# Performance work log

Measured on AMD Instinct MI355X. Metric: run time of the kernel, lower is better.

Reference implementation:

```python
import jax, jax.numpy as jnp
import numpy as np
import math

B, T, C, H = 2, 2048, 1024, 16
D = C // H
EPS = 1e-5

def _layer_norm(x, w, b):
    m = jnp.mean(x, axis=-1, keepdims=True)
    v = jnp.mean((x - m) ** 2, axis=-1, keepdims=True)
    return (x - m) * jax.lax.rsqrt(v + EPS) * w + b

def setup_inputs() -> dict:
    key = jax.random.key(0)
    ks = jax.random.split(key, 8)
    s_attn = 1.0 / math.sqrt(C)
    s_fc = 1.0 / math.sqrt(C)
    s_fc2 = 1.0 / math.sqrt(4 * C)
    return {
        "x": jax.random.normal(ks[0], (B, T, C), dtype=jnp.float32),
        "ln1_w": jnp.ones((C,), jnp.float32),
        "ln1_b": jnp.zeros((C,), jnp.float32),
        "w_qkv": jax.random.normal(ks[1], (C, 3 * C), jnp.float32) * s_attn,  # [in,out]
        "b_qkv": jnp.zeros((3 * C,), jnp.float32),
        "w_proj": jax.random.normal(ks[2], (C, C), jnp.float32) * s_attn,
        "b_proj": jnp.zeros((C,), jnp.float32),
        "ln2_w": jnp.ones((C,), jnp.float32),
        "ln2_b": jnp.zeros((C,), jnp.float32),
        "w_fc": jax.random.normal(ks[3], (C, 4 * C), jnp.float32) * s_fc,
        "b_fc": jnp.zeros((4 * C,), jnp.float32),
        "w_fc2": jax.random.normal(ks[4], (4 * C, C), jnp.float32) * s_fc2,
        "b_fc2": jnp.zeros((C,), jnp.float32),
    }

def reference(x, ln1_w, ln1_b, w_qkv, b_qkv, w_proj, b_proj,
              ln2_w, ln2_b, w_fc, b_fc, w_fc2, b_fc2):
    # --- attention branch ---
    h = _layer_norm(x, ln1_w, ln1_b)
    qkv = h @ w_qkv + b_qkv                      # [B,T,3C]
    q, k, v = jnp.split(qkv, 3, axis=-1)
    # [B,T,C] -> [B,H,T,D]
    q = q.reshape(B, T, H, D).transpose(0, 2, 1, 3)
    k = k.reshape(B, T, H, D).transpose(0, 2, 1, 3)
    v = v.reshape(B, T, H, D).transpose(0, 2, 1, 3)
    scale = 1.0 / math.sqrt(D)
    scores = jnp.einsum("bhtd,bhsd->bhts", q, k) * scale  # [B,H,T,T]
    causal = jnp.tril(jnp.ones((T, T), dtype=bool))
    scores = jnp.where(causal, scores, -jnp.inf)
    attn_w = jax.nn.softmax(scores, axis=-1)     # dropout_p = 0.0
    attn_out = jnp.einsum("bhts,bhsd->bhtd", attn_w, v)
    attn_out = attn_out.transpose(0, 2, 1, 3).reshape(B, T, C)
    attn_out = attn_out @ w_proj + b_proj
    x = x + attn_out
    # --- MLP branch ---
    h2 = _layer_norm(x, ln2_w, ln2_b)
    h2 = jax.nn.gelu(h2 @ w_fc + b_fc, approximate=False)
    x = x + (h2 @ w_fc2 + b_fc2)
    return x, jnp.mean(attn_w, axis=0)           # ([B,T,C], [H,T,T])
```

## Files before the change

### kernel.cpp

```cpp
#include <hip/hip_runtime.h>
#include <cmath>

#define BB 2
#define TT 2048
#define CC 1024
#define HH 16
#define DD 64

typedef unsigned short u16;
typedef __attribute__((ext_vector_type(8))) short bf16x8;
typedef __attribute__((ext_vector_type(4))) float f32x4;

__device__ __forceinline__ u16 f2bf(float f) {
    union { float f; unsigned u; } v; v.f = f;
    return (u16)((v.u + 0x7fff + ((v.u >> 16) & 1)) >> 16);
}

__device__ __forceinline__ float bf2f(u16 h) {
    union { unsigned u; float f; } v; v.u = ((unsigned)h) << 16;
    return v.f;
}

__device__ __forceinline__ float gelu_exact(float v) {
    return 0.5f * v * (1.0f + erff(v * 0.70710678118654752440f));
}

__device__ __forceinline__ void glds16(const void* g, void* l) {
    __builtin_amdgcn_global_load_lds(
        (const __attribute__((address_space(1))) void*)g,
        (__attribute__((address_space(3))) void*)l, 16, 0, 0);
}

__global__ __launch_bounds__(256) void wcvt_kernel(const float* __restrict__ W,
                                                   u16* __restrict__ WT,
                                                   int K, int N) {
    __shared__ u16 t[64][65];
    const int n0 = blockIdx.x * 64, k0 = blockIdx.y * 64;
    const int tid = threadIdx.x;
    const int c = tid & 63;
#pragma unroll
    for (int it = 0; it < 16; ++it) {
        int r = it * 4 + (tid >> 6);
        t[c][r] = f2bf(W[(size_t)(k0 + r) * N + n0 + c]);
    }
    __syncthreads();
#pragma unroll
    for (int it = 0; it < 16; ++it) {
        int r = it * 4 + (tid >> 6);
        WT[(size_t)(n0 + r) * K + k0 + c] = t[r][c];
    }
}

__global__ __launch_bounds__(256) void ln_kernel(const float* __restrict__ x,
                                                 const float* __restrict__ w,
                                                 const float* __restrict__ b,
                                                 u16* __restrict__ out) {
    const int row = blockIdx.x;
    const int tid = threadIdx.x;
    const float* xr = x + (size_t)row * CC;
    u16* orow = out + (size_t)row * CC;

    __shared__ float red[256];

    float v[4];
#pragma unroll
    for (int i = 0; i < 4; ++i) v[i] = xr[tid + i * 256];

    red[tid] = v[0] + v[1] + v[2] + v[3];
    __syncthreads();
    for (int off = 128; off > 0; off >>= 1) {
        if (tid < off) red[tid] += red[tid + off];
        __syncthreads();
    }
    const float mean = red[0] * (1.0f / CC);
    __syncthreads();

    float d[4], sq = 0.f;
#pragma unroll
    for (int i = 0; i < 4; ++i) { d[i] = v[i] - mean; sq += d[i] * d[i]; }
    red[tid] = sq;
    __syncthreads();
    for (int off = 128; off > 0; off >>= 1) {
        if (tid < off) red[tid] += red[tid + off];
        __syncthreads();
    }
    const float rstd = rsqrtf(red[0] * (1.0f / CC) + 1e-5f);

#pragma unroll
    for (int i = 0; i < 4; ++i) {
        int c = tid + i * 256;
        orow[c] = f2bf(d[i] * rstd * w[c] + b[c]);
    }
}

template <int EPI, int OUTBF, int WM, int WN, int FI, int FJ>
__global__ __launch_bounds__(256) void gemm_mfma(const u16* __restrict__ A,
                                                 const u16* __restrict__ BT,
                                                 const float* __restrict__ bias,
                                                 const float* __restrict__ res,
                                                 void* __restrict__ out,
                                                 int M, int N, int K) {
    constexpr int TM = WM * FI * 16;
    constexpr int TN = WN * FJ * 16;
    __shared__ u16 As[TM * 32];
    __shared__ u16 Bs[TN * 32];

    const int tid = threadIdx.x;
    const int lane = tid & 63;
    const int w = tid >> 6;
    const int wr = w / WN, wc = w % WN;
    const int m16 = lane & 15;
    const int quad = lane >> 4;

    const int bm = blockIdx.y * TM;
    const int bn = blockIdx.x * TN;

    f32x4 acc[FI][FJ] = {};

    for (int k0 = 0; k0 < K; k0 += 32) {
#pragma unroll
        for (int it = 0; it < TM / 64; ++it) {
            int cb = w * (TM / 64) * 64 + it * 64;
            int q = cb + lane;
            glds16(&A[(size_t)(bm + (q >> 2)) * K + k0 + (q & 3) * 8], &As[cb * 8]);
        }
#pragma unroll
        for (int it = 0; it < TN / 64; ++it) {
            int cb = w * (TN / 64) * 64 + it * 64;
            int q = cb + lane;
            glds16(&BT[(size_t)(bn + (q >> 2)) * K + k0 + (q & 3) * 8], &Bs[cb * 8]);
        }
        __syncthreads();

        bf16x8 a[FI], b[FJ];
#pragma unroll
        for (int i = 0; i < FI; ++i)
            a[i] = *(const bf16x8*)&As[(wr * FI * 16 + 16 * i + m16) * 32 + quad * 8];
#pragma unroll
        for (int j = 0; j < FJ; ++j)
            b[j] = *(const bf16x8*)&Bs[(wc * FJ * 16 + 16 * j + m16) * 32 + quad * 8];
#pragma unroll
        for (int i = 0; i < FI; ++i)
#pragma unroll
            for (int j = 0; j < FJ; ++j)
                acc[i][j] = __builtin_amdgcn_mfma_f32_16x16x32_bf16(a[i], b[j], acc[i][j], 0, 0, 0);
        __syncthreads();
    }

#pragma unroll
    for (int i = 0; i < FI; ++i) {
        const int row = bm + wr * FI * 16 + 16 * i + quad * 4;
#pragma unroll
        for (int j = 0; j < FJ; ++j) {
            const int col = bn + wc * FJ * 16 + 16 * j + m16;
            const float bv = bias[col];
#pragma unroll
            for (int r = 0; r < 4; ++r) {
                float v = acc[i][j][r] + bv;
                if (EPI == 1) v = gelu_exact(v);
                if (EPI == 2) v += res[(size_t)(row + r) * N + col];
                if (OUTBF) ((u16*)out)[(size_t)(row + r) * N + col] = f2bf(v);
                else ((float*)out)[(size_t)(row + r) * N + col] = v;
            }
        }
    }
}

__global__ __launch_bounds__(256) void attn_kernel(const float* __restrict__ qkv,
                                                   float* __restrict__ attn_mean,
                                                   u16* __restrict__ attn_out) {
    const int lid = blockIdx.x;
    const int u = lid & 255;
    const int h = u & 15;
    const int ta = u >> 4;
    const int tt = (lid < 256) ? ta : 31 - ta;
    const int t0 = tt * 64;

    const int tid = threadIdx.x;
    const int lane = tid & 63;
    const int w = tid >> 6;
    const int m16 = lane & 15;
    const int quad = lane >> 4;
    const size_t TC3 = 3 * CC;

    __shared__ u16 Qh[2][64][64];
    __shared__ u16 Ql[2][64][64];
    __shared__ u16 Kh[64][64];
    __shared__ u16 Kl[64][64];
    __shared__ u16 VT[64][64];
    __shared__ u16 Ps[64][64];

    const int arow = w * 16 + m16;
    const int sw = (m16 & 7) << 3;
    const int rbase = w * 16 + quad * 4;

    auto stage_hilo = [&](const float* src, u16 (*Hd)[64], u16 (*Ld)[64], float scale) {
#pragma unroll
        for (int it = 0; it < 4; ++it) {
            int e = tid + it * 256;
            int s = e >> 4, c4 = e & 15;
            float4 v = *reinterpret_cast<const float4*>(src + (size_t)s * TC3 + c4 * 4);
            float fv[4] = {v.x * scale, v.y * scale, v.z * scale, v.w * scale};
            u16 hh[4], ll[4];
#pragma unroll
            for (int i = 0; i < 4; ++i) {
                union { float f; unsigned u; } tbits; tbits.f = fv[i];
                hh[i] = (u16)(tbits.u >> 16);
                ll[i] = f2bf(fv[i] - bf2f(hh[i]));
            }
            int col = (c4 * 4) ^ ((s & 7) << 3);
            *reinterpret_cast<ushort4*>(&Hd[s][col]) = make_ushort4(hh[0], hh[1], hh[2], hh[3]);
            *reinterpret_cast<ushort4*>(&Ld[s][col]) = make_ushort4(ll[0], ll[1], ll[2], ll[3]);
        }
    };

    auto stage_vt = [&](const float* src) {
#pragma unroll
        for (int it = 0; it < 4; ++it) {
            int e = tid + it * 256;
            int s = e >> 4, c4 = e & 15;
            float4 v = *reinterpret_cast<const float4*>(src + (size_t)s * TC3 + c4 * 4);
            float fv[4] = {v.x, v.y, v.z, v.w};
#pragma unroll
            for (int i = 0; i < 4; ++i) {
                int d = c4 * 4 + i;
                VT[d][s ^ ((d & 7) << 3)] = f2bf(fv[i]);
            }
        }
    };

    auto compute_S = [&](int b, f32x4 (&acc)[4], bool diag) {
#pragma unroll
        for (int ks = 0; ks < 2; ++ks) {
            const int acol = (ks * 32 + quad * 8) ^ sw;
            bf16x8 ah = *(const bf16x8*)&Qh[b][arow][acol];
            bf16x8 al = *(const bf16x8*)&Ql[b][arow][acol];
#pragma unroll
            for (int j = 0; j < 4; ++j) {
                bf16x8 bh = *(const bf16x8*)&Kh[j * 16 + m16][acol];
                bf16x8 bl = *(const bf16x8*)&Kl[j * 16 + m16][acol];
                acc[j] = __builtin_amdgcn_mfma_f32_16x16x32_bf16(ah, bh, acc[j], 0, 0, 0);
                acc[j] = __builtin_amdgcn_mfma_f32_16x16x32_bf16(al, bh, acc[j], 0, 0, 0);
                acc[j] = __builtin_amdgcn_mfma_f32_16x16x32_bf16(ah, bl, acc[j], 0, 0, 0);
            }
        }
        if (diag) {
#pragma unroll
            for (int j = 0; j < 4; ++j)
#pragma unroll
                for (int r = 0; r < 4; ++r)
                    if (j * 16 + m16 > rbase + r) acc[j][r] = -INFINITY;
        }
    };

    auto pv_acc = [&](f32x4 (&O)[4]) {
#pragma unroll
        for (int ks = 0; ks < 2; ++ks) {
            const int ko = (ks * 32 + quad * 8) ^ sw;
            bf16x8 a = *(const bf16x8*)&Ps[arow][ko];
#pragma unroll
            for (int j = 0; j < 4; ++j) {
                bf16x8 bv = *(const bf16x8*)&VT[j * 16 + m16][ko];
                O[j] = __builtin_amdgcn_mfma_f32_16x16x32_bf16(a, bv, O[j], 0, 0, 0);
            }
        }
    };

    stage_hilo(qkv + (size_t)t0 * TC3 + h * DD, Qh[0], Ql[0], 0.125f);
    stage_hilo(qkv + (size_t)TT * TC3 + (size_t)t0 * TC3 + h * DD, Qh[1], Ql[1], 0.125f);

    float m_b[2][4], l_b[2][4];
#pragma unroll
    for (int b = 0; b < 2; ++b) {
        float m_r[4] = {-INFINITY, -INFINITY, -INFINITY, -INFINITY};
        float l_r[4] = {0.f, 0.f, 0.f, 0.f};
        const float* kbase = qkv + (size_t)b * TT * TC3 + CC + h * DD;
        for (int st = 0; st <= tt; ++st) {
            __syncthreads();
            stage_hilo(kbase + (size_t)st * 64 * TC3, Kh, Kl, 1.0f);
            __syncthreads();
            f32x4 acc[4] = {};
            compute_S(b, acc, st == tt);
#pragma unroll
            for (int r = 0; r < 4; ++r) {
                float t = fmaxf(fmaxf(acc[0][r], acc[1][r]), fmaxf(acc[2][r], acc[3][r]));
                t = fmaxf(t, __shfl_xor(t, 1));
                t = fmaxf(t, __shfl_xor(t, 2));
                t = fmaxf(t, __shfl_xor(t, 4));
                t = fmaxf(t, __shfl_xor(t, 8));
                const float mn = fmaxf(m_r[r], t);
                float sum = __expf(acc[0][r] - mn) + __expf(acc[1][r] - mn) +
                            __expf(acc[2][r] - mn) + __expf(acc[3][r] - mn);
                sum += __shfl_xor(sum, 1);
                sum += __shfl_xor(sum, 2);
                sum += __shfl_xor(sum, 4);
                sum += __shfl_xor(sum, 8);
                l_r[r] = l_r[r] * __expf(m_r[r] - mn) + sum;
                m_r[r] = mn;
            }
        }
#pragma unroll
        for (int r = 0; r < 4; ++r) { m_b[b][r] = m_r[r]; l_b[b][r] = 1.0f / l_r[r]; }
    }

    f32x4 O0[4] = {}, O1[4] = {};
    const float* k0base = qkv + CC + h * DD;
    const float* k1base = qkv + (size_t)TT * TC3 + CC + h * DD;
    const float* v0base = qkv + 2 * CC + h * DD;
    const float* v1base = qkv + (size_t)TT * TC3 + 2 * CC + h * DD;

    for (int st = 0; st <= tt; ++st) {
        const int s0 = st * 64;
        const bool diag = (st == tt);
        float P0[4][4], P1[4][4];

        __syncthreads();
        stage_hilo(k0base + (size_t)s0 * TC3, Kh, Kl, 1.0f);
        __syncthreads();
        {
            f32x4 acc[4] = {};
            compute_S(0, acc, diag);
#pragma unroll
            for (int j = 0; j < 4; ++j)
#pragma unroll
                for (int r = 0; r < 4; ++r)
                    P0[j][r] = __expf(acc[j][r] - m_b[0][r]) * l_b[0][r];
        }
        __syncthreads();
        stage_hilo(k1base + (size_t)s0 * TC3, Kh, Kl, 1.0f);
        __syncthreads();
        {
            f32x4 acc[4] = {};
            compute_S(1, acc, diag);
#pragma unroll
            for (int j = 0; j < 4; ++j)
#pragma unroll
                for (int r = 0; r < 4; ++r)
                    P1[j][r] = __expf(acc[j][r] - m_b[1][r]) * l_b[1][r];
        }
#pragma unroll
        for (int r = 0; r < 4; ++r) {
            float* mrow = attn_mean + ((size_t)h * TT + t0 + rbase + r) * TT + s0;
#pragma unroll
            for (int j = 0; j < 4; ++j)
                mrow[j * 16 + m16] = 0.5f * (P0[j][r] + P1[j][r]);
        }
#pragma unroll
        for (int r = 0; r < 4; ++r) {
            const int prow = rbase + r;
            const int psw = (prow & 7) << 3;
#pragma unroll
            for (int j = 0; j < 4; ++j)
                Ps[prow][(j * 16 + m16) ^ psw] = f2bf(P0[j][r]);
        }
        stage_vt(v0base + (size_t)s0 * TC3);
        __syncthreads();
        pv_acc(O0);
        __syncthreads();
#pragma unroll
        for (int r = 0; r < 4; ++r) {
            const int prow = rbase + r;
            const int psw = (prow & 7) << 3;
#pragma unroll
            for (int j = 0; j < 4; ++j)
                Ps[prow][(j * 16 + m16) ^ psw] = f2bf(P1[j][r]);
        }
        stage_vt(v1base + (size_t)s0 * TC3);
        __syncthreads();
        pv_acc(O1);
    }

#pragma unroll
    for (int r = 0; r < 4; ++r) {
        const int trow = t0 + rbase + r;
#pragma unroll
        for (int j = 0; j < 4; ++j) {
            attn_out[((size_t)0 * TT + trow) * CC + h * DD + j * 16 + m16] = f2bf(O0[j][r]);
            attn_out[((size_t)1 * TT + trow) * CC + h * DD + j * 16 + m16] = f2bf(O1[j][r]);
        }
    }

    const int c0 = (tt + 1) * 64;
    const float4 z4 = make_float4(0.f, 0.f, 0.f, 0.f);
    for (int r = 0; r < 64; ++r) {
        float* row = attn_mean + ((size_t)h * TT + t0 + r) * TT;
        for (int c = c0 + tid * 4; c < TT; c += 1024)
            *reinterpret_cast<float4*>(row + c) = z4;
    }
}

extern "C" void kernel_launch(void* const* d_in, const int* in_sizes, int n_in,
                              void* d_out, int out_size, void* d_ws, size_t ws_size,
                              hipStream_t stream) {
    const float* x      = (const float*)d_in[0];
    const float* ln1_w  = (const float*)d_in[1];
    const float* ln1_b  = (const float*)d_in[2];
    const float* w_qkv  = (const float*)d_in[3];
    const float* b_qkv  = (const float*)d_in[4];
    const float* w_proj = (const float*)d_in[5];
    const float* b_proj = (const float*)d_in[6];
    const float* ln2_w  = (const float*)d_in[7];
    const float* ln2_b  = (const float*)d_in[8];
    const float* w_fc   = (const float*)d_in[9];
    const float* b_fc   = (const float*)d_in[10];
    const float* w_fc2  = (const float*)d_in[11];
    const float* b_fc2  = (const float*)d_in[12];

    float* out_x    = (float*)d_out;
    float* out_attn = out_x + (size_t)BB * TT * CC;

    char* wp = (char*)d_ws;
    u16* wT_qkv = (u16*)wp;  wp += (size_t)3072 * 1024 * 2;
    u16* wT_proj = (u16*)wp; wp += (size_t)1024 * 1024 * 2;
    u16* wT_fc  = (u16*)wp;  wp += (size_t)4096 * 1024 * 2;
    u16* wT_fc2 = (u16*)wp;  wp += (size_t)1024 * 4096 * 2;
    u16* h_ln   = (u16*)wp;  wp += (size_t)4096 * 1024 * 2;
    u16* att_o  = (u16*)wp;  wp += (size_t)4096 * 1024 * 2;
    u16* h2     = (u16*)wp;  wp += (size_t)4096 * 4096 * 2;
    float* qkv  = (float*)wp; wp += (size_t)4096 * 3072 * 4;
    float* x1   = (float*)wp; wp += (size_t)4096 * 1024 * 4;

    const int M = BB * TT;

    wcvt_kernel<<<dim3(3072 / 64, 1024 / 64), 256, 0, stream>>>(w_qkv, wT_qkv, 1024, 3072);
    wcvt_kernel<<<dim3(1024 / 64, 1024 / 64), 256, 0, stream>>>(w_proj, wT_proj, 1024, 1024);
    wcvt_kernel<<<dim3(4096 / 64, 1024 / 64), 256, 0, stream>>>(w_fc, wT_fc, 1024, 4096);
    wcvt_kernel<<<dim3(1024 / 64, 4096 / 64), 256, 0, stream>>>(w_fc2, wT_fc2, 4096, 1024);

    ln_kernel<<<M, 256, 0, stream>>>(x, ln1_w, ln1_b, h_ln);
    gemm_mfma<0, 0, 2, 2, 4, 4><<<dim3(3072 / 128, M / 128), 256, 0, stream>>>(
        h_ln, wT_qkv, b_qkv, nullptr, qkv, M, 3072, 1024);
    attn_kernel<<<512, 256, 0, stream>>>(qkv, out_attn, att_o);
    gemm_mfma<2, 0, 4, 1, 2, 4><<<dim3(1024 / 64, M / 128), 256, 0, stream>>>(
        att_o, wT_proj, b_proj, x, x1, M, 1024, 1024);
    ln_kernel<<<M, 256, 0, stream>>>(x1, ln2_w, ln2_b, h_ln);
    gemm_mfma<1, 1, 2, 2, 4, 4><<<dim3(4096 / 128, M / 128), 256, 0, stream>>>(
        h_ln, wT_fc, b_fc, nullptr, h2, M, 4096, 1024);
    gemm_mfma<2, 0, 4, 1, 2, 4><<<dim3(1024 / 64, M / 128), 256, 0, stream>>>(
        h2, wT_fc2, b_fc2, x1, out_x, M, 1024, 4096);
}
```

Before: 788.4 us.

## Pre-convert K/V tiles to bf16 in a separate kernel and stream them via direct-to-LDS loads

New measurement: 719.0 us. 1.1x faster.

```diff
diff --git a/kernel.cpp b/kernel.cpp
--- a/kernel.cpp
+++ b/kernel.cpp
@@ -166,7 +166,61 @@
     }
 }
 
+__global__ __launch_bounds__(256) void qkvcvt_kernel(const float* __restrict__ qkv,
+                                                     u16* __restrict__ Khg,
+                                                     u16* __restrict__ Klg,
+                                                     u16* __restrict__ VTg) {
+    const int idx = blockIdx.x;
+    const int st = idx & 31;
+    const int h = (idx >> 5) & 15;
+    const int b = idx >> 9;
+    const int tid = threadIdx.x;
+    const size_t TC3 = 3 * CC;
+
+    const float* kbase = qkv + (size_t)b * TT * TC3 + (size_t)st * 64 * TC3 + CC + h * DD;
+    const float* vbase = kbase + CC;
+    u16* kh = Khg + (size_t)idx * 4096;
+    u16* kl = Klg + (size_t)idx * 4096;
+    u16* vt = VTg + (size_t)idx * 4096;
+
+    __shared__ u16 lvt[64][65];
+
+#pragma unroll
+    for (int it = 0; it < 4; ++it) {
+        int e = tid + it * 256;
+        int s = e >> 4, c4 = e & 15;
+        float4 v = *reinterpret_cast<const float4*>(kbase + (size_t)s * TC3 + c4 * 4);
+        float fv[4] = {v.x, v.y, v.z, v.w};
+        u16 hh[4], ll[4];
+#pragma unroll
+        for (int i = 0; i < 4; ++i) {
+            union { float f; unsigned u; } tb; tb.f = fv[i];
+            hh[i] = (u16)(tb.u >> 16);
+            ll[i] = f2bf(fv[i] - bf2f(hh[i]));
+        }
+        int col = (c4 * 4) ^ ((s & 7) << 3);
+        *reinterpret_cast<ushort4*>(&kh[s * 64 + col]) = make_ushort4(hh[0], hh[1], hh[2], hh[3]);
+        *reinterpret_cast<ushort4*>(&kl[s * 64 + col]) = make_ushort4(ll[0], ll[1], ll[2], ll[3]);
+        float4 vv = *reinterpret_cast<const float4*>(vbase + (size_t)s * TC3 + c4 * 4);
+        lvt[c4 * 4 + 0][s] = f2bf(vv.x);
+        lvt[c4 * 4 + 1][s] = f2bf(vv.y);
+        lvt[c4 * 4 + 2][s] = f2bf(vv.z);
+        lvt[c4 * 4 + 3][s] = f2bf(vv.w);
+    }
+    __syncthreads();
+#pragma unroll
+    for (int it = 0; it < 4; ++it) {
+        int e = tid + it * 256;
+        int d = e >> 4, s4 = (e & 15) * 4;
+        ushort4 o = make_ushort4(lvt[d][s4], lvt[d][s4 + 1], lvt[d][s4 + 2], lvt[d][s4 + 3]);
+        *reinterpret_cast<ushort4*>(&vt[d * 64 + (s4 ^ ((d & 7) << 3))]) = o;
+    }
+}
+
 __global__ __launch_bounds__(256) void attn_kernel(const float* __restrict__ qkv,
+                                                   const u16* __restrict__ Khg,
+                                                   const u16* __restrict__ Klg,
+                                                   const u16* __restrict__ VTg,
                                                    float* __restrict__ attn_mean,
                                                    u16* __restrict__ attn_out) {
     const int lid = blockIdx.x;
@@ -183,65 +237,58 @@
     const int quad = lane >> 4;
     const size_t TC3 = 3 * CC;
 
-    __shared__ u16 Qh[2][64][64];
-    __shared__ u16 Ql[2][64][64];
-    __shared__ u16 Kh[64][64];
-    __shared__ u16 Kl[64][64];
-    __shared__ u16 VT[64][64];
-    __shared__ u16 Ps[64][64];
+    __shared__ u16 Ks[2][2][64][64];
+    __shared__ u16 VTs[2][64][64];
 
     const int arow = w * 16 + m16;
     const int sw = (m16 & 7) << 3;
     const int rbase = w * 16 + quad * 4;
 
-    auto stage_hilo = [&](const float* src, u16 (*Hd)[64], u16 (*Ld)[64], float scale) {
-#pragma unroll
-        for (int it = 0; it < 4; ++it) {
-            int e = tid + it * 256;
-            int s = e >> 4, c4 = e & 15;
-            float4 v = *reinterpret_cast<const float4*>(src + (size_t)s * TC3 + c4 * 4);
-            float fv[4] = {v.x * scale, v.y * scale, v.z * scale, v.w * scale};
-            u16 hh[4], ll[4];
-#pragma unroll
-            for (int i = 0; i < 4; ++i) {
-                union { float f; unsigned u; } tbits; tbits.f = fv[i];
-                hh[i] = (u16)(tbits.u >> 16);
-                ll[i] = f2bf(fv[i] - bf2f(hh[i]));
-            }
-            int col = (c4 * 4) ^ ((s & 7) << 3);
-            *reinterpret_cast<ushort4*>(&Hd[s][col]) = make_ushort4(hh[0], hh[1], hh[2], hh[3]);
-            *reinterpret_cast<ushort4*>(&Ld[s][col]) = make_ushort4(ll[0], ll[1], ll[2], ll[3]);
-        }
+    auto toff = [&](int b, int st) -> size_t {
+        return ((size_t)((b * 16 + h) * 32 + st)) * 4096;
     };
 
-    auto stage_vt = [&](const float* src) {
-#pragma unroll
-        for (int it = 0; it < 4; ++it) {
-            int e = tid + it * 256;
-            int s = e >> 4, c4 = e & 15;
-            float4 v = *reinterpret_cast<const float4*>(src + (size_t)s * TC3 + c4 * 4);
-            float fv[4] = {v.x, v.y, v.z, v.w};
-#pragma unroll
-            for (int i = 0; i < 4; ++i) {
-                int d = c4 * 4 + i;
-                VT[d][s ^ ((d & 7) << 3)] = f2bf(fv[i]);
-            }
-        }
+    auto stage_tile = [&](const u16* g, u16* l) {
+        glds16(g + w * 1024 + lane * 8, l + w * 1024);
+        glds16(g + w * 1024 + 512 + lane * 8, l + w * 1024 + 512);
     };
 
-    auto compute_S = [&](int b, f32x4 (&acc)[4], bool diag) {
+    bf16x8 qh[2][2], ql[2][2];
+#pragma unroll
+    for (int b = 0; b < 2; ++b) {
+        const float* qp = qkv + (size_t)b * TT * TC3 + (size_t)(t0 + arow) * TC3 + h * DD;
 #pragma unroll
         for (int ks = 0; ks < 2; ++ks) {
-            const int acol = (ks * 32 + quad * 8) ^ sw;
-            bf16x8 ah = *(const bf16x8*)&Qh[b][arow][acol];
-            bf16x8 al = *(const bf16x8*)&Ql[b][arow][acol];
+            float4 v0 = *reinterpret_cast<const float4*>(qp + ks * 32 + quad * 8);
+            float4 v1 = *reinterpret_cast<const float4*>(qp + ks * 32 + quad * 8 + 4);
+            float f[8] = {v0.x, v0.y, v0.z, v0.w, v1.x, v1.y, v1.z, v1.w};
+            union { bf16x8 v; u16 s[8]; } H, L;
+#pragma unroll
+            for (int i = 0; i < 8; ++i) {
+                float fv = f[i] * 0.125f;
+                union { float f; unsigned u; } tb; tb.f = fv;
+                u16 hh = (u16)(tb.u >> 16);
+                H.s[i] = hh;
+                L.s[i] = f2bf(fv - bf2f(hh));
+            }
+            qh[b][ks] = H.v;
+            ql[b][ks] = L.v;
+        }
+    }
+
+    auto compute_S = [&](const bf16x8 (&QH)[2], const bf16x8 (&QL)[2],
+                         const u16 (*KH)[64], const u16 (*KL)[64],
+                         f32x4 (&acc)[4], bool diag) {
+#pragma unroll
+        for (int ks = 0; ks < 2; ++ks) {
 #pragma unroll
             for (int j = 0; j < 4; ++j) {
-                bf16x8 bh = *(const bf16x8*)&Kh[j * 16 + m16][acol];
-                bf16x8 bl = *(const bf16x8*)&Kl[j * 16 + m16][acol];
-                acc[j] = __builtin_amdgcn_mfma_f32_16x16x32_bf16(ah, bh, acc[j], 0, 0, 0);
-                acc[j] = __builtin_amdgcn_mfma_f32_16x16x32_bf16(al, bh, acc[j], 0, 0, 0);
-                acc[j] = __builtin_amdgcn_mfma_f32_16x16x32_bf16(ah, bl, acc[j], 0, 0, 0);
+                const int co = (ks * 32 + quad * 8) ^ sw;
+                bf16x8 bh = *(const bf16x8*)&KH[j * 16 + m16][co];
+                bf16x8 bl = *(const bf16x8*)&KL[j * 16 + m16][co];
+                acc[j] = __builtin_amdgcn_mfma_f32_16x16x32_bf16(QH[ks], bh, acc[j], 0, 0, 0);
+                acc[j] = __builtin_amdgcn_mfma_f32_16x16x32_bf16(QL[ks], bh, acc[j], 0, 0, 0);
+                acc[j] = __builtin_amdgcn_mfma_f32_16x16x32_bf16(QH[ks], bl, acc[j], 0, 0, 0);
             }
         }
         if (diag) {
@@ -253,34 +300,37 @@
         }
     };
 
-    auto pv_acc = [&](f32x4 (&O)[4]) {
+    auto pv_acc = [&](f32x4 (&O)[4], const u16 (*Ps)[64], const u16 (*VT)[64]) {
 #pragma unroll
         for (int ks = 0; ks < 2; ++ks) {
-            const int ko = (ks * 32 + quad * 8) ^ sw;
-            bf16x8 a = *(const bf16x8*)&Ps[arow][ko];
+            const int co = (ks * 32 + quad * 8) ^ sw;
+            bf16x8 a = *(const bf16x8*)&Ps[arow][co];
 #pragma unroll
             for (int j = 0; j < 4; ++j) {
-                bf16x8 bv = *(const bf16x8*)&VT[j * 16 + m16][ko];
+                bf16x8 bv = *(const bf16x8*)&VT[j * 16 + m16][co];
                 O[j] = __builtin_amdgcn_mfma_f32_16x16x32_bf16(a, bv, O[j], 0, 0, 0);
             }
         }
     };
 
-    stage_hilo(qkv + (size_t)t0 * TC3 + h * DD, Qh[0], Ql[0], 0.125f);
-    stage_hilo(qkv + (size_t)TT * TC3 + (size_t)t0 * TC3 + h * DD, Qh[1], Ql[1], 0.125f);
-
-    float m_b[2][4], l_b[2][4];
-#pragma unroll
-    for (int b = 0; b < 2; ++b) {
-        float m_r[4] = {-INFINITY, -INFINITY, -INFINITY, -INFINITY};
-        float l_r[4] = {0.f, 0.f, 0.f, 0.f};
-        const float* kbase = qkv + (size_t)b * TT * TC3 + CC + h * DD;
-        for (int st = 0; st <= tt; ++st) {
-            __syncthreads();
-            stage_hilo(kbase + (size_t)st * 64 * TC3, Kh, Kl, 1.0f);
-            __syncthreads();
+    float m_r[2][4], l_r[2][4];
+#pragma unroll
+    for (int b = 0; b < 2; ++b)
+#pragma unroll
+        for (int r = 0; r < 4; ++r) { m_r[b][r] = -INFINITY; l_r[b][r] = 0.f; }
+
+    for (int st = 0; st <= tt; ++st) {
+        __syncthreads();
+        stage_tile(Khg + toff(0, st), &Ks[0][0][0][0]);
+        stage_tile(Klg + toff(0, st), &Ks[0][1][0][0]);
+        stage_tile(Khg + toff(1, st), &Ks[1][0][0][0]);
+        stage_tile(Klg + toff(1, st), &Ks[1][1][0][0]);
+        __syncthreads();
+        const bool diag = (st == tt);
+#pragma unroll
+        for (int b = 0; b < 2; ++b) {
             f32x4 acc[4] = {};
-            compute_S(b, acc, st == tt);
+            compute_S(qh[b], ql[b], Ks[b][0], Ks[b][1], acc, diag);
 #pragma unroll
             for (int r = 0; r < 4; ++r) {
                 float t = fmaxf(fmaxf(acc[0][r], acc[1][r]), fmaxf(acc[2][r], acc[3][r]));
@@ -288,86 +338,70 @@
                 t = fmaxf(t, __shfl_xor(t, 2));
                 t = fmaxf(t, __shfl_xor(t, 4));
                 t = fmaxf(t, __shfl_xor(t, 8));
-                const float mn = fmaxf(m_r[r], t);
-                float sum = __expf(acc[0][r] - mn) + __expf(acc[1][r] - mn) +
-                            __expf(acc[2][r] - mn) + __expf(acc[3][r] - mn);
-                sum += __shfl_xor(sum, 1);
-                sum += __shfl_xor(sum, 2);
-                sum += __shfl_xor(sum, 4);
-                sum += __shfl_xor(sum, 8);
-                l_r[r] = l_r[r] * __expf(m_r[r] - mn) + sum;
-                m_r[r] = mn;
-            }
-        }
-#pragma unroll
-        for (int r = 0; r < 4; ++r) { m_b[b][r] = m_r[r]; l_b[b][r] = 1.0f / l_r[r]; }
-    }
+                const float mn = fmaxf(m_r[b][r], t);
+                float s = __expf(acc[0][r] - mn) + __expf(acc[1][r] - mn) +
+                          __expf(acc[2][r] - mn) + __expf(acc[3][r] - mn);
+                s += __shfl_xor(s, 1);
+                s += __shfl_xor(s, 2);
+                s += __shfl_xor(s, 4);
+                s += __shfl_xor(s, 8);
+                l_r[b][r] = l_r[b][r] * __expf(m_r[b][r] - mn) + s;
+                m_r[b][r] = mn;
+            }
+        }
+    }
+#pragma unroll
+    for (int b = 0; b < 2; ++b)
+#pragma unroll
+        for (int r = 0; r < 4; ++r) l_r[b][r] = 1.0f / l_r[b][r];
 
     f32x4 O0[4] = {}, O1[4] = {};
-    const float* k0base = qkv + CC + h * DD;
-    const float* k1base = qkv + (size_t)TT * TC3 + CC + h * DD;
-    const float* v0base = qkv + 2 * CC + h * DD;
-    const float* v1base = qkv + (size_t)TT * TC3 + 2 * CC + h * DD;
-
     for (int st = 0; st <= tt; ++st) {
         const int s0 = st * 64;
         const bool diag = (st == tt);
-        float P0[4][4], P1[4][4];
-
-        __syncthreads();
-        stage_hilo(k0base + (size_t)s0 * TC3, Kh, Kl, 1.0f);
-        __syncthreads();
-        {
-            f32x4 acc[4] = {};
-            compute_S(0, acc, diag);
-#pragma unroll
-            for (int j = 0; j < 4; ++j)
-#pragma unroll
-                for (int r = 0; r < 4; ++r)
-                    P0[j][r] = __expf(acc[j][r] - m_b[0][r]) * l_b[0][r];
-        }
-        __syncthreads();
-        stage_hilo(k1base + (size_t)s0 * TC3, Kh, Kl, 1.0f);
-        __syncthreads();
-        {
-            f32x4 acc[4] = {};
-            compute_S(1, acc, diag);
-#pragma unroll
-            for (int j = 0; j < 4; ++j)
-#pragma unroll
-                for (int r = 0; r < 4; ++r)
-                    P1[j][r] = __expf(acc[j][r] - m_b[1][r]) * l_b[1][r];
-        }
+        __syncthreads();
+        stage_tile(Khg + toff(0, st), &Ks[0][0][0][0]);
+        stage_tile(Klg + toff(0, st), &Ks[0][1][0][0]);
+        stage_tile(Khg + toff(1, st), &Ks[1][0][0][0]);
+        stage_tile(Klg + toff(1, st), &Ks[1][1][0][0]);
+        stage_tile(VTg + toff(0, st), &VTs[0][0][0]);
+        stage_tile(VTg + toff(1, st), &VTs[1][0][0]);
+        __syncthreads();
+
+        f32x4 a0[4] = {}, a1[4] = {};
+        compute_S(qh[0], ql[0], Ks[0][0], Ks[0][1], a0, diag);
+        compute_S(qh[1], ql[1], Ks[1][0], Ks[1][1], a1, diag);
+
+#pragma unroll
+        for (int j = 0; j < 4; ++j)
+#pragma unroll
+            for (int r = 0; r < 4; ++r) {
+                a0[j][r] = __expf(a0[j][r] - m_r[0][r]) * l_r[0][r];
+                a1[j][r] = __expf(a1[j][r] - m_r[1][r]) * l_r[1][r];
+            }
+
 #pragma unroll
         for (int r = 0; r < 4; ++r) {
             float* mrow = attn_mean + ((size_t)h * TT + t0 + rbase + r) * TT + s0;
 #pragma unroll
             for (int j = 0; j < 4; ++j)
-                mrow[j * 16 + m16] = 0.5f * (P0[j][r] + P1[j][r]);
-        }
+                mrow[j * 16 + m16] = 0.5f * (a0[j][r] + a1[j][r]);
+        }
+
+        __syncthreads();
+
 #pragma unroll
         for (int r = 0; r < 4; ++r) {
             const int prow = rbase + r;
             const int psw = (prow & 7) << 3;
 #pragma unroll
-            for (int j = 0; j < 4; ++j)
-                Ps[prow][(j * 16 + m16) ^ psw] = f2bf(P0[j][r]);
-        }
-        stage_vt(v0base + (size_t)s0 * TC3);
-        __syncthreads();
-        pv_acc(O0);
-        __syncthreads();
-#pragma unroll
-        for (int r = 0; r < 4; ++r) {
-            const int prow = rbase + r;
-            const int psw = (prow & 7) << 3;
-#pragma unroll
-            for (int j = 0; j < 4; ++j)
-                Ps[prow][(j * 16 + m16) ^ psw] = f2bf(P1[j][r]);
-        }
-        stage_vt(v1base + (size_t)s0 * TC3);
-        __syncthreads();
-        pv_acc(O1);
+            for (int j = 0; j < 4; ++j) {
+                Ks[0][0][prow][(j * 16 + m16) ^ psw] = f2bf(a0[j][r]);
+                Ks[1][0][prow][(j * 16 + m16) ^ psw] = f2bf(a1[j][r]);
+            }
+        }
+        pv_acc(O0, Ks[0][0], VTs[0]);
+        pv_acc(O1, Ks[1][0], VTs[1]);
     }
 
 #pragma unroll
@@ -420,6 +454,10 @@
     float* qkv  = (float*)wp; wp += (size_t)4096 * 3072 * 4;
     float* x1   = (float*)wp; wp += (size_t)4096 * 1024 * 4;
 
+    u16* Khg = h2;
+    u16* Klg = Khg + (size_t)1024 * 4096;
+    u16* VTg = Klg + (size_t)1024 * 4096;
+
     const int M = BB * TT;
 
     wcvt_kernel<<<dim3(3072 / 64, 1024 / 64), 256, 0, stream>>>(w_qkv, wT_qkv, 1024, 3072);
@@ -430,7 +468,8 @@
     ln_kernel<<<M, 256, 0, stream>>>(x, ln1_w, ln1_b, h_ln);
     gemm_mfma<0, 0, 2, 2, 4, 4><<<dim3(3072 / 128, M / 128), 256, 0, stream>>>(
         h_ln, wT_qkv, b_qkv, nullptr, qkv, M, 3072, 1024);
-    attn_kernel<<<512, 256, 0, stream>>>(qkv, out_attn, att_o);
+    qkvcvt_kernel<<<1024, 256, 0, stream>>>(qkv, Khg, Klg, VTg);
+    attn_kernel<<<512, 256, 0, stream>>>(qkv, Khg, Klg, VTg, out_attn, att_o);
     gemm_mfma<2, 0, 4, 1, 2, 4><<<dim3(1024 / 64, M / 128), 256, 0, stream>>>(
         att_o, wT_proj, b_proj, x, x1, M, 1024, 1024);
     ln_kernel<<<M, 256, 0, stream>>>(x1, ln2_w, ln2_b, h_ln);
```
